# Kernel tuning notes

Hardware: AMD Instinct MI355X
Metric: run time of the kernel (lower is better)

## Reference

```python
import jax, jax.numpy as jnp
import numpy as np

N = 8192
D_IN = 32
HIDDEN = [32, 32, 32]   # -> 2 GraphConvolution layers
FC = [32, 1]            # hfc = [32, 32, 1] -> 2 Linear layers


def _uniform(key, shape, stdv):
    return jax.random.uniform(key, shape, jnp.float32, -stdv, stdv)


def setup_inputs() -> dict:
    key = jax.random.key(0)
    ks = jax.random.split(key, 32)
    inp = {}
    inp["V"] = jax.random.normal(ks[0], (N, D_IN), jnp.float32)
    inp["adj"] = jax.random.randint(ks[1], (N, N), 0, 4, jnp.int32)
    # GCN layer params: w1, w2, w3 [in, out], bias [out]; init U(-stdv, stdv), stdv = 1/sqrt(out)
    ki = 2
    for li in range(len(HIDDEN) - 1):
        a, b = HIDDEN[li], HIDDEN[li + 1]
        stdv = 1.0 / np.sqrt(b)
        for wname in ("w1", "w2", "w3"):
            inp[f"{wname}_{li}"] = _uniform(ks[ki], (a, b), stdv); ki += 1
        inp[f"gb_{li}"] = _uniform(ks[ki], (b,), stdv); ki += 1
    # FC params (torch Linear default init: U(-1/sqrt(in), 1/sqrt(in)))
    hfc = [HIDDEN[-1]] + FC
    for li in range(len(hfc) - 1):
        a, b = hfc[li], hfc[li + 1]
        stdv = 1.0 / np.sqrt(a)
        inp[f"fcW_{li}"] = _uniform(ks[ki], (b, a), stdv); ki += 1  # torch Linear weight is [out, in]
        inp[f"fcb_{li}"] = _uniform(ks[ki], (b,), stdv); ki += 1
    return inp


def _gcn(V, adj, w1, w2, w3, bias):
    # masked-adjacency relational aggregation: sum_k (adj==k) @ (V @ w_k)
    dt = V.dtype
    o = (adj == 1).astype(dt) @ (V @ w1)
    o = o + (adj == 2).astype(dt) @ (V @ w2)
    o = o + (adj == 3).astype(dt) @ (V @ w3)
    return jax.nn.relu(o + bias)


def reference(V, adj, w1_0, w2_0, w3_0, gb_0, w1_1, w2_1, w3_1, gb_1,
              fcW_0, fcb_0, fcW_1, fcb_1):
    Z = _gcn(V, adj, w1_0, w2_0, w3_0, gb_0)          # [N, 32]
    Z = _gcn(Z, adj, w1_1, w2_1, w3_1, gb_1)          # [N, 32]
    Z = jnp.sum(Z, axis=0)                             # [32] sum pooling over nodes
    Z = jax.nn.relu(Z @ fcW_0.T + fcb_0)               # dropout = identity (eval mode)
    Z = Z @ fcW_1.T + fcb_1                            # [1]
    return jax.nn.sigmoid(Z)
```

## Files before the change

kernel.cpp:

```cpp
#include <hip/hip_runtime.h>
#include <cmath>

#define NN 8192

typedef _Float16 half8 __attribute__((ext_vector_type(8)));
typedef float floatx4 __attribute__((ext_vector_type(4)));
typedef unsigned int uint;

template <int L2>
__global__ __launch_bounds__(256) void h_kernel(
    const float* __restrict__ X, const float* __restrict__ w1,
    const float* __restrict__ w2, const float* __restrict__ w3,
    const float* __restrict__ gbias, _Float16* __restrict__ Hfrag) {
  __shared__ float wl[32][32];
  __shared__ float Xs[64][32];
  const int tid = threadIdx.x;
  const int ch = blockIdx.y;
  const float* wsrc = (ch == 0) ? w1 : (ch == 1) ? w2 : w3;
  for (int i = tid; i < 1024; i += 256) ((float*)wl)[i] = wsrc[i];
  const size_t base = (size_t)blockIdx.x * 2048 + tid * 8;
  if (L2 == 0) {
    float4 x0 = ((const float4*)(X + base))[0];
    float4 x1 = ((const float4*)(X + base))[1];
    *((float4*)(&Xs[0][0] + tid * 8)) = x0;
    *((float4*)(&Xs[0][0] + tid * 8 + 4)) = x1;
  } else {
    float4 s0 = {0.f, 0.f, 0.f, 0.f}, s1 = {0.f, 0.f, 0.f, 0.f};
#pragma unroll
    for (int c = 0; c < 8; ++c) {
      const float4* p = (const float4*)(X + (size_t)c * NN * 32 + base);
      float4 a = p[0], b = p[1];
      s0.x += a.x; s0.y += a.y; s0.z += a.z; s0.w += a.w;
      s1.x += b.x; s1.y += b.y; s1.z += b.z; s1.w += b.w;
    }
    const int c0 = (tid * 8) & 31;
    const float4 b0 = *(const float4*)(gbias + c0);
    const float4 b1 = *(const float4*)(gbias + c0 + 4);
    s0.x += b0.x; s0.y += b0.y; s0.z += b0.z; s0.w += b0.w;
    s1.x += b1.x; s1.y += b1.y; s1.z += b1.z; s1.w += b1.w;
    s0.x = s0.x > 0.f ? s0.x : 0.f; s0.y = s0.y > 0.f ? s0.y : 0.f;
    s0.z = s0.z > 0.f ? s0.z : 0.f; s0.w = s0.w > 0.f ? s0.w : 0.f;
    s1.x = s1.x > 0.f ? s1.x : 0.f; s1.y = s1.y > 0.f ? s1.y : 0.f;
    s1.z = s1.z > 0.f ? s1.z : 0.f; s1.w = s1.w > 0.f ? s1.w : 0.f;
    *((float4*)(&Xs[0][0] + tid * 8)) = s0;
    *((float4*)(&Xs[0][0] + tid * 8 + 4)) = s1;
  }
  __syncthreads();
  const int n = tid & 31, jb = tid >> 5;
  const int j0 = blockIdx.x * 64 + jb * 8;
  const int t = j0 >> 5;
  const int lane = (n & 15) | (((j0 & 31) >> 3) << 4);
  const int tile = n >> 4;
  half8 hv;
#pragma unroll
  for (int jj = 0; jj < 8; ++jj) {
    const float4* xr = (const float4*)(&Xs[jb * 8 + jj][0]);
    float acc = 0.f;
#pragma unroll
    for (int d4 = 0; d4 < 8; ++d4) {
      float4 x = xr[d4];
      acc += x.x * wl[d4 * 4 + 0][n];
      acc += x.y * wl[d4 * 4 + 1][n];
      acc += x.z * wl[d4 * 4 + 2][n];
      acc += x.w * wl[d4 * 4 + 3][n];
    }
    hv[jj] = (_Float16)acc;
  }
  size_t idx = ((((size_t)ch * 256 + t) * 2 + tile) * 64 + lane) * 8;
  *(half8*)(Hfrag + idx) = hv;
}

__device__ __forceinline__ void agg_phaseB(const uint* ptile, float* red_raw,
                                           const half8* __restrict__ Hf,
                                           float* __restrict__ Zpart, int rg,
                                           int c, int tid) {
  const int w = tid >> 6, lane = tid & 63;
  const int m = lane & 15, q = lane >> 4;
  uint mk[8];
  *(uint4*)(mk) = *(const uint4*)(ptile + (w * 2) * 256 + lane * 4);
  *(uint4*)(mk + 4) = *(const uint4*)(ptile + (w * 2 + 1) * 256 + lane * 4);
  __syncthreads();
  floatx4 acc00 = {0.f, 0.f, 0.f, 0.f}, acc01 = {0.f, 0.f, 0.f, 0.f};
  floatx4 acc10 = {0.f, 0.f, 0.f, 0.f}, acc11 = {0.f, 0.f, 0.f, 0.f};
#pragma unroll 2
  for (int tl = 0; tl < 8; ++tl) {
    const int t = c * 32 + w * 8 + tl;
    const size_t hb = (size_t)t * 128 + lane;
    half8 b00 = Hf[hb],          b01 = Hf[hb + 64];
    half8 b10 = Hf[hb + 32768],  b11 = Hf[hb + 32768 + 64];
    half8 b20 = Hf[hb + 65536],  b21 = Hf[hb + 65536 + 64];
    const uint pk = mk[tl];
    half8 a1r0, a2r0, a3r0, a1r1, a2r1, a3r1;
#pragma unroll
    for (int i = 0; i < 8; ++i) {
      const int p0 = (pk >> (2 * i)) & 3;
      const int p1 = (pk >> (16 + 2 * i)) & 3;
      a1r0[i] = (p0 == 1) ? (_Float16)1.f : (_Float16)0.f;
      a2r0[i] = (p0 == 2) ? (_Float16)1.f : (_Float16)0.f;
      a3r0[i] = (p0 == 3) ? (_Float16)1.f : (_Float16)0.f;
      a1r1[i] = (p1 == 1) ? (_Float16)1.f : (_Float16)0.f;
      a2r1[i] = (p1 == 2) ? (_Float16)1.f : (_Float16)0.f;
      a3r1[i] = (p1 == 3) ? (_Float16)1.f : (_Float16)0.f;
    }
    acc00 = __builtin_amdgcn_mfma_f32_16x16x32_f16(a1r0, b00, acc00, 0, 0, 0);
    acc00 = __builtin_amdgcn_mfma_f32_16x16x32_f16(a2r0, b10, acc00, 0, 0, 0);
    acc00 = __builtin_amdgcn_mfma_f32_16x16x32_f16(a3r0, b20, acc00, 0, 0, 0);
    acc01 = __builtin_amdgcn_mfma_f32_16x16x32_f16(a1r0, b01, acc01, 0, 0, 0);
    acc01 = __builtin_amdgcn_mfma_f32_16x16x32_f16(a2r0, b11, acc01, 0, 0, 0);
    acc01 = __builtin_amdgcn_mfma_f32_16x16x32_f16(a3r0, b21, acc01, 0, 0, 0);
    acc10 = __builtin_amdgcn_mfma_f32_16x16x32_f16(a1r1, b00, acc10, 0, 0, 0);
    acc10 = __builtin_amdgcn_mfma_f32_16x16x32_f16(a2r1, b10, acc10, 0, 0, 0);
    acc10 = __builtin_amdgcn_mfma_f32_16x16x32_f16(a3r1, b20, acc10, 0, 0, 0);
    acc11 = __builtin_amdgcn_mfma_f32_16x16x32_f16(a1r1, b01, acc11, 0, 0, 0);
    acc11 = __builtin_amdgcn_mfma_f32_16x16x32_f16(a2r1, b11, acc11, 0, 0, 0);
    acc11 = __builtin_amdgcn_mfma_f32_16x16x32_f16(a3r1, b21, acc11, 0, 0, 0);
  }
  float (*red)[4][64][4] = (float (*)[4][64][4])red_raw;
#pragma unroll
  for (int r = 0; r < 4; ++r) {
    red[w][0][lane][r] = acc00[r];
    red[w][1][lane][r] = acc01[r];
    red[w][2][lane][r] = acc10[r];
    red[w][3][lane][r] = acc11[r];
  }
  __syncthreads();
  if (w == 0) {
    const int rbase = rg * 32;
#pragma unroll
    for (int r = 0; r < 4; ++r) {
      const float c00 = red[0][0][lane][r] + red[1][0][lane][r] +
                        red[2][0][lane][r] + red[3][0][lane][r];
      const float c01 = red[0][1][lane][r] + red[1][1][lane][r] +
                        red[2][1][lane][r] + red[3][1][lane][r];
      const float c10 = red[0][2][lane][r] + red[1][2][lane][r] +
                        red[2][2][lane][r] + red[3][2][lane][r];
      const float c11 = red[0][3][lane][r] + red[1][3][lane][r] +
                        red[2][3][lane][r] + red[3][3][lane][r];
      const int ro0 = rbase + q * 4 + r;
      float* zp0 = Zpart + ((size_t)c * NN + ro0) * 32;
      zp0[m] = c00;
      zp0[16 + m] = c01;
      float* zp1 = Zpart + ((size_t)c * NN + ro0 + 16) * 32;
      zp1[m] = c10;
      zp1[16 + m] = c11;
    }
  }
}

__global__ __launch_bounds__(256, 8) void agg_kernel(
    const int* __restrict__ adj, const half8* __restrict__ Hf,
    float* __restrict__ Zpart) {
  __shared__ char smraw[16384];
  uint* ptile = (uint*)smraw;
  const int tid = threadIdx.x;
  const int rg = blockIdx.x >> 3, c = blockIdx.x & 7;
  const int tg = tid >> 5;
  const int qt = (tid >> 1) & 3;
  const int t4 = (tid >> 3) & 3;
  const int ih = tid & 1;
  const int byte_base = tg * 1024 + qt * 256 + t4 * 4 + ih;
  unsigned char* pb = (unsigned char*)ptile;
  const size_t gofs = (size_t)rg * 32 * NN + c * 1024 + tid * 4;
#pragma unroll
  for (int r0 = 0; r0 < 32; r0 += 8) {
    int4 a[8];
#pragma unroll
    for (int rr = 0; rr < 8; ++rr)
      a[rr] = *(const int4*)(adj + gofs + (size_t)(r0 + rr) * NN);
#pragma unroll
    for (int rr = 0; rr < 8; ++rr) {
      const int r = r0 + rr;
      const uint b = (uint)(a[rr].x & 3) | ((uint)(a[rr].y & 3) << 2) |
                     ((uint)(a[rr].z & 3) << 4) | ((uint)(a[rr].w & 3) << 6);
      pb[byte_base + (r & 15) * 16 + (r >> 4) * 2] = (unsigned char)b;
    }
  }
  __syncthreads();
  agg_phaseB(ptile, (float*)smraw, Hf, Zpart, rg, c, tid);
}

__global__ __launch_bounds__(256) void pool_kernel(
    const float* __restrict__ Zpart, const float* __restrict__ bias,
    float* __restrict__ partials) {
  const int tid = threadIdx.x;
  const int col = tid & 31, ro = tid >> 5;
  const float b = bias[col];
  float s = 0.f;
  for (int rr = 0; rr < 32; ++rr) {
    const size_t r = (size_t)blockIdx.x * 256 + ro * 32 + rr;
    float v = b;
#pragma unroll
    for (int c = 0; c < 8; ++c) v += Zpart[(size_t)c * NN * 32 + r * 32 + col];
    s += v > 0.f ? v : 0.f;
  }
  __shared__ float red[8][32];
  red[ro][col] = s;
  __syncthreads();
  if (tid < 32) {
    float t = 0.f;
#pragma unroll
    for (int i = 0; i < 8; ++i) t += red[i][tid];
    partials[(size_t)blockIdx.x * 32 + tid] = t;
  }
}

__global__ __launch_bounds__(256) void fc_kernel(
    const float* __restrict__ partials, int np, const float* __restrict__ W0,
    const float* __restrict__ b0, const float* __restrict__ W1,
    const float* __restrict__ b1, float* __restrict__ out) {
  __shared__ float acc8[8][32];
  __shared__ float z[32], y[32];
  const int tid = threadIdx.x;
  const int col = tid & 31, ch = tid >> 5;
  float s = 0.f;
  for (int i = ch; i < np; i += 8) s += partials[(size_t)i * 32 + col];
  acc8[ch][col] = s;
  __syncthreads();
  if (tid < 32) {
    float t = 0.f;
#pragma unroll
    for (int i = 0; i < 8; ++i) t += acc8[i][tid];
    z[tid] = t;
  }
  __syncthreads();
  if (tid < 32) {
    float acc = b0[tid];
    for (int n = 0; n < 32; ++n) acc += W0[tid * 32 + n] * z[n];
    y[tid] = acc > 0.f ? acc : 0.f;
  }
  __syncthreads();
  if (tid == 0) {
    float acc = b1[0];
    for (int mm = 0; mm < 32; ++mm) acc += W1[mm] * y[mm];
    out[0] = 1.f / (1.f + expf(-acc));
  }
}

extern "C" void kernel_launch(void* const* d_in, const int* in_sizes, int n_in,
                              void* d_out, int out_size, void* d_ws,
                              size_t ws_size, hipStream_t stream) {
  const float* V   = (const float*)d_in[0];
  const int*   adj = (const int*)d_in[1];
  const float *w10 = (const float*)d_in[2], *w20 = (const float*)d_in[3],
              *w30 = (const float*)d_in[4], *gb0 = (const float*)d_in[5];
  const float *w11 = (const float*)d_in[6], *w21 = (const float*)d_in[7],
              *w31 = (const float*)d_in[8], *gb1 = (const float*)d_in[9];
  const float *fW0 = (const float*)d_in[10], *fb0 = (const float*)d_in[11],
              *fW1 = (const float*)d_in[12], *fb1 = (const float*)d_in[13];
  float* out = (float*)d_out;
  char* ws = (char*)d_ws;

  _Float16* Hfrag    = (_Float16*)ws;
  float*    Zpart    = (float*)(ws + 1572864);
  float*    partials = (float*)(ws + 9961472);

  h_kernel<0><<<dim3(128, 3), 256, 0, stream>>>(V, w10, w20, w30, nullptr,
                                                Hfrag);
  agg_kernel<<<2048, 256, 0, stream>>>(adj, (const half8*)Hfrag, Zpart);
  h_kernel<1><<<dim3(128, 3), 256, 0, stream>>>(Zpart, w11, w21, w31, gb0,
                                                Hfrag);
  agg_kernel<<<2048, 256, 0, stream>>>(adj, (const half8*)Hfrag, Zpart);
  pool_kernel<<<32, 256, 0, stream>>>(Zpart, gb1, partials);
  fc_kernel<<<1, 256, 0, stream>>>(partials, 32, fW0, fb0, fW1, fb1, out);
}
```

Measured before the change: 487.1 us.

## Pack adjacency once in first aggregation and reuse packed masks in second layer

```diff
diff --git a/kernel.cpp b/kernel.cpp
--- a/kernel.cpp
+++ b/kernel.cpp
@@ -70,25 +70,28 @@
   *(half8*)(Hfrag + idx) = hv;
 }
 
-__device__ __forceinline__ void agg_phaseB(const uint* ptile, float* red_raw,
-                                           const half8* __restrict__ Hf,
-                                           float* __restrict__ Zpart, int rg,
-                                           int c, int tid) {
+__device__ __forceinline__ void phaseB_core(const uint* mk,
+                                            const half8* __restrict__ Hf,
+                                            float* red_raw,
+                                            float* __restrict__ Zpart, int rg,
+                                            int c, int tid) {
   const int w = tid >> 6, lane = tid & 63;
   const int m = lane & 15, q = lane >> 4;
-  uint mk[8];
-  *(uint4*)(mk) = *(const uint4*)(ptile + (w * 2) * 256 + lane * 4);
-  *(uint4*)(mk + 4) = *(const uint4*)(ptile + (w * 2 + 1) * 256 + lane * 4);
-  __syncthreads();
+  const half8* hp = Hf + (size_t)(c * 32 + w * 8) * 128 + lane;
+  half8 b00 = hp[0],     b01 = hp[64];
+  half8 b10 = hp[32768], b11 = hp[32768 + 64];
+  half8 b20 = hp[65536], b21 = hp[65536 + 64];
   floatx4 acc00 = {0.f, 0.f, 0.f, 0.f}, acc01 = {0.f, 0.f, 0.f, 0.f};
   floatx4 acc10 = {0.f, 0.f, 0.f, 0.f}, acc11 = {0.f, 0.f, 0.f, 0.f};
-#pragma unroll 2
+#pragma unroll
   for (int tl = 0; tl < 8; ++tl) {
-    const int t = c * 32 + w * 8 + tl;
-    const size_t hb = (size_t)t * 128 + lane;
-    half8 b00 = Hf[hb],          b01 = Hf[hb + 64];
-    half8 b10 = Hf[hb + 32768],  b11 = Hf[hb + 32768 + 64];
-    half8 b20 = Hf[hb + 65536],  b21 = Hf[hb + 65536 + 64];
+    half8 n00, n01, n10, n11, n20, n21;
+    if (tl < 7) {
+      const half8* np = hp + (tl + 1) * 128;
+      n00 = np[0];     n01 = np[64];
+      n10 = np[32768]; n11 = np[32768 + 64];
+      n20 = np[65536]; n21 = np[65536 + 64];
+    }
     const uint pk = mk[tl];
     half8 a1r0, a2r0, a3r0, a1r1, a2r1, a3r1;
 #pragma unroll
@@ -114,6 +117,9 @@
     acc11 = __builtin_amdgcn_mfma_f32_16x16x32_f16(a1r1, b01, acc11, 0, 0, 0);
     acc11 = __builtin_amdgcn_mfma_f32_16x16x32_f16(a2r1, b11, acc11, 0, 0, 0);
     acc11 = __builtin_amdgcn_mfma_f32_16x16x32_f16(a3r1, b21, acc11, 0, 0, 0);
+    if (tl < 7) {
+      b00 = n00; b01 = n01; b10 = n10; b11 = n11; b20 = n20; b21 = n21;
+    }
   }
   float (*red)[4][64][4] = (float (*)[4][64][4])red_raw;
 #pragma unroll
@@ -147,9 +153,9 @@
   }
 }
 
-__global__ __launch_bounds__(256, 8) void agg_kernel(
-    const int* __restrict__ adj, const half8* __restrict__ Hf,
-    float* __restrict__ Zpart) {
+__global__ __launch_bounds__(256, 4) void agg1_kernel(
+    const int* __restrict__ adj, uint* __restrict__ packed_g,
+    const half8* __restrict__ Hf, float* __restrict__ Zpart) {
   __shared__ char smraw[16384];
   uint* ptile = (uint*)smraw;
   const int tid = threadIdx.x;
@@ -176,7 +182,30 @@
     }
   }
   __syncthreads();
-  agg_phaseB(ptile, (float*)smraw, Hf, Zpart, rg, c, tid);
+  uint* pg = packed_g + (size_t)blockIdx.x * 2048;
+  *(uint4*)(pg + tid * 8) = *(const uint4*)(ptile + tid * 8);
+  *(uint4*)(pg + tid * 8 + 4) = *(const uint4*)(ptile + tid * 8 + 4);
+  const int w = tid >> 6, lane = tid & 63;
+  uint mk[8];
+  *(uint4*)(mk) = *(const uint4*)(ptile + (w * 2) * 256 + lane * 4);
+  *(uint4*)(mk + 4) = *(const uint4*)(ptile + (w * 2 + 1) * 256 + lane * 4);
+  __syncthreads();
+  phaseB_core(mk, Hf, (float*)smraw, Zpart, rg, c, tid);
+}
+
+__global__ __launch_bounds__(256, 4) void agg2_kernel(
+    const uint* __restrict__ packed_g, const half8* __restrict__ Hf,
+    float* __restrict__ Zpart) {
+  __shared__ float red_lds[4][4][64][4];
+  const int tid = threadIdx.x;
+  const int rg = blockIdx.x >> 3, c = blockIdx.x & 7;
+  const int w = tid >> 6, lane = tid & 63;
+  const uint* pg =
+      packed_g + (size_t)blockIdx.x * 2048 + (w * 2) * 256 + lane * 4;
+  uint mk[8];
+  *(uint4*)(mk) = *(const uint4*)(pg);
+  *(uint4*)(mk + 4) = *(const uint4*)(pg + 256);
+  phaseB_core(mk, Hf, (float*)red_lds, Zpart, rg, c, tid);
 }
 
 __global__ __launch_bounds__(256) void pool_kernel(
@@ -253,13 +282,15 @@
   _Float16* Hfrag    = (_Float16*)ws;
   float*    Zpart    = (float*)(ws + 1572864);
   float*    partials = (float*)(ws + 9961472);
+  uint*     packed   = (uint*)(ws + 10223616);
 
   h_kernel<0><<<dim3(128, 3), 256, 0, stream>>>(V, w10, w20, w30, nullptr,
                                                 Hfrag);
-  agg_kernel<<<2048, 256, 0, stream>>>(adj, (const half8*)Hfrag, Zpart);
+  agg1_kernel<<<2048, 256, 0, stream>>>(adj, packed, (const half8*)Hfrag,
+                                        Zpart);
   h_kernel<1><<<dim3(128, 3), 256, 0, stream>>>(Zpart, w11, w21, w31, gb0,
                                                 Hfrag);
-  agg_kernel<<<2048, 256, 0, stream>>>(adj, (const half8*)Hfrag, Zpart);
+  agg2_kernel<<<2048, 256, 0, stream>>>(packed, (const half8*)Hfrag, Zpart);
   pool_kernel<<<32, 256, 0, stream>>>(Zpart, gb1, partials);
   fc_kernel<<<1, 256, 0, stream>>>(partials, 32, fW0, fb0, fW1, fb1, out);
 }
```

Result: faster. 440.4 us (-9.6%).

## Pack adjacency once to 2-bit global buffer and reuse it across both GCN layers

Applied to the files above, without the earlier changes.

```diff
diff --git a/kernel.cpp b/kernel.cpp
--- a/kernel.cpp
+++ b/kernel.cpp
@@ -7,11 +7,10 @@
 typedef float floatx4 __attribute__((ext_vector_type(4)));
 typedef unsigned int uint;
 
-template <int L2>
 __global__ __launch_bounds__(256) void h_kernel(
     const float* __restrict__ X, const float* __restrict__ w1,
     const float* __restrict__ w2, const float* __restrict__ w3,
-    const float* __restrict__ gbias, _Float16* __restrict__ Hfrag) {
+    _Float16* __restrict__ Hfrag) {
   __shared__ float wl[32][32];
   __shared__ float Xs[64][32];
   const int tid = threadIdx.x;
@@ -19,38 +18,16 @@
   const float* wsrc = (ch == 0) ? w1 : (ch == 1) ? w2 : w3;
   for (int i = tid; i < 1024; i += 256) ((float*)wl)[i] = wsrc[i];
   const size_t base = (size_t)blockIdx.x * 2048 + tid * 8;
-  if (L2 == 0) {
-    float4 x0 = ((const float4*)(X + base))[0];
-    float4 x1 = ((const float4*)(X + base))[1];
-    *((float4*)(&Xs[0][0] + tid * 8)) = x0;
-    *((float4*)(&Xs[0][0] + tid * 8 + 4)) = x1;
-  } else {
-    float4 s0 = {0.f, 0.f, 0.f, 0.f}, s1 = {0.f, 0.f, 0.f, 0.f};
-#pragma unroll
-    for (int c = 0; c < 8; ++c) {
-      const float4* p = (const float4*)(X + (size_t)c * NN * 32 + base);
-      float4 a = p[0], b = p[1];
-      s0.x += a.x; s0.y += a.y; s0.z += a.z; s0.w += a.w;
-      s1.x += b.x; s1.y += b.y; s1.z += b.z; s1.w += b.w;
-    }
-    const int c0 = (tid * 8) & 31;
-    const float4 b0 = *(const float4*)(gbias + c0);
-    const float4 b1 = *(const float4*)(gbias + c0 + 4);
-    s0.x += b0.x; s0.y += b0.y; s0.z += b0.z; s0.w += b0.w;
-    s1.x += b1.x; s1.y += b1.y; s1.z += b1.z; s1.w += b1.w;
-    s0.x = s0.x > 0.f ? s0.x : 0.f; s0.y = s0.y > 0.f ? s0.y : 0.f;
-    s0.z = s0.z > 0.f ? s0.z : 0.f; s0.w = s0.w > 0.f ? s0.w : 0.f;
-    s1.x = s1.x > 0.f ? s1.x : 0.f; s1.y = s1.y > 0.f ? s1.y : 0.f;
-    s1.z = s1.z > 0.f ? s1.z : 0.f; s1.w = s1.w > 0.f ? s1.w : 0.f;
-    *((float4*)(&Xs[0][0] + tid * 8)) = s0;
-    *((float4*)(&Xs[0][0] + tid * 8 + 4)) = s1;
-  }
+  float4 x0 = ((const float4*)(X + base))[0];
+  float4 x1 = ((const float4*)(X + base))[1];
+  *((float4*)(&Xs[0][0] + tid * 8)) = x0;
+  *((float4*)(&Xs[0][0] + tid * 8 + 4)) = x1;
   __syncthreads();
   const int n = tid & 31, jb = tid >> 5;
   const int j0 = blockIdx.x * 64 + jb * 8;
   const int t = j0 >> 5;
   const int lane = (n & 15) | (((j0 & 31) >> 3) << 4);
-  const int tile = n >> 4;
+  const int h = n >> 4;
   half8 hv;
 #pragma unroll
   for (int jj = 0; jj < 8; ++jj) {
@@ -66,92 +43,13 @@
     }
     hv[jj] = (_Float16)acc;
   }
-  size_t idx = ((((size_t)ch * 256 + t) * 2 + tile) * 64 + lane) * 8;
+  size_t idx = ((((size_t)ch * 256 + t) * 2 + h) * 64 + lane) * 8;
   *(half8*)(Hfrag + idx) = hv;
 }
 
-__device__ __forceinline__ void agg_phaseB(const uint* ptile, float* red_raw,
-                                           const half8* __restrict__ Hf,
-                                           float* __restrict__ Zpart, int rg,
-                                           int c, int tid) {
-  const int w = tid >> 6, lane = tid & 63;
-  const int m = lane & 15, q = lane >> 4;
-  uint mk[8];
-  *(uint4*)(mk) = *(const uint4*)(ptile + (w * 2) * 256 + lane * 4);
-  *(uint4*)(mk + 4) = *(const uint4*)(ptile + (w * 2 + 1) * 256 + lane * 4);
-  __syncthreads();
-  floatx4 acc00 = {0.f, 0.f, 0.f, 0.f}, acc01 = {0.f, 0.f, 0.f, 0.f};
-  floatx4 acc10 = {0.f, 0.f, 0.f, 0.f}, acc11 = {0.f, 0.f, 0.f, 0.f};
-#pragma unroll 2
-  for (int tl = 0; tl < 8; ++tl) {
-    const int t = c * 32 + w * 8 + tl;
-    const size_t hb = (size_t)t * 128 + lane;
-    half8 b00 = Hf[hb],          b01 = Hf[hb + 64];
-    half8 b10 = Hf[hb + 32768],  b11 = Hf[hb + 32768 + 64];
-    half8 b20 = Hf[hb + 65536],  b21 = Hf[hb + 65536 + 64];
-    const uint pk = mk[tl];
-    half8 a1r0, a2r0, a3r0, a1r1, a2r1, a3r1;
-#pragma unroll
-    for (int i = 0; i < 8; ++i) {
-      const int p0 = (pk >> (2 * i)) & 3;
-      const int p1 = (pk >> (16 + 2 * i)) & 3;
-      a1r0[i] = (p0 == 1) ? (_Float16)1.f : (_Float16)0.f;
-      a2r0[i] = (p0 == 2) ? (_Float16)1.f : (_Float16)0.f;
-      a3r0[i] = (p0 == 3) ? (_Float16)1.f : (_Float16)0.f;
-      a1r1[i] = (p1 == 1) ? (_Float16)1.f : (_Float16)0.f;
-      a2r1[i] = (p1 == 2) ? (_Float16)1.f : (_Float16)0.f;
-      a3r1[i] = (p1 == 3) ? (_Float16)1.f : (_Float16)0.f;
-    }
-    acc00 = __builtin_amdgcn_mfma_f32_16x16x32_f16(a1r0, b00, acc00, 0, 0, 0);
-    acc00 = __builtin_amdgcn_mfma_f32_16x16x32_f16(a2r0, b10, acc00, 0, 0, 0);
-    acc00 = __builtin_amdgcn_mfma_f32_16x16x32_f16(a3r0, b20, acc00, 0, 0, 0);
-    acc01 = __builtin_amdgcn_mfma_f32_16x16x32_f16(a1r0, b01, acc01, 0, 0, 0);
-    acc01 = __builtin_amdgcn_mfma_f32_16x16x32_f16(a2r0, b11, acc01, 0, 0, 0);
-    acc01 = __builtin_amdgcn_mfma_f32_16x16x32_f16(a3r0, b21, acc01, 0, 0, 0);
-    acc10 = __builtin_amdgcn_mfma_f32_16x16x32_f16(a1r1, b00, acc10, 0, 0, 0);
-    acc10 = __builtin_amdgcn_mfma_f32_16x16x32_f16(a2r1, b10, acc10, 0, 0, 0);
-    acc10 = __builtin_amdgcn_mfma_f32_16x16x32_f16(a3r1, b20, acc10, 0, 0, 0);
-    acc11 = __builtin_amdgcn_mfma_f32_16x16x32_f16(a1r1, b01, acc11, 0, 0, 0);
-    acc11 = __builtin_amdgcn_mfma_f32_16x16x32_f16(a2r1, b11, acc11, 0, 0, 0);
-    acc11 = __builtin_amdgcn_mfma_f32_16x16x32_f16(a3r1, b21, acc11, 0, 0, 0);
-  }
-  float (*red)[4][64][4] = (float (*)[4][64][4])red_raw;
-#pragma unroll
-  for (int r = 0; r < 4; ++r) {
-    red[w][0][lane][r] = acc00[r];
-    red[w][1][lane][r] = acc01[r];
-    red[w][2][lane][r] = acc10[r];
-    red[w][3][lane][r] = acc11[r];
-  }
-  __syncthreads();
-  if (w == 0) {
-    const int rbase = rg * 32;
-#pragma unroll
-    for (int r = 0; r < 4; ++r) {
-      const float c00 = red[0][0][lane][r] + red[1][0][lane][r] +
-                        red[2][0][lane][r] + red[3][0][lane][r];
-      const float c01 = red[0][1][lane][r] + red[1][1][lane][r] +
-                        red[2][1][lane][r] + red[3][1][lane][r];
-      const float c10 = red[0][2][lane][r] + red[1][2][lane][r] +
-                        red[2][2][lane][r] + red[3][2][lane][r];
-      const float c11 = red[0][3][lane][r] + red[1][3][lane][r] +
-                        red[2][3][lane][r] + red[3][3][lane][r];
-      const int ro0 = rbase + q * 4 + r;
-      float* zp0 = Zpart + ((size_t)c * NN + ro0) * 32;
-      zp0[m] = c00;
-      zp0[16 + m] = c01;
-      float* zp1 = Zpart + ((size_t)c * NN + ro0 + 16) * 32;
-      zp1[m] = c10;
-      zp1[16 + m] = c11;
-    }
-  }
-}
-
-__global__ __launch_bounds__(256, 8) void agg_kernel(
-    const int* __restrict__ adj, const half8* __restrict__ Hf,
-    float* __restrict__ Zpart) {
-  __shared__ char smraw[16384];
-  uint* ptile = (uint*)smraw;
+__global__ __launch_bounds__(256, 8) void pack_kernel(
+    const int* __restrict__ adj, uint* __restrict__ packed_g) {
+  __shared__ uint ptile[2048];
   const int tid = threadIdx.x;
   const int rg = blockIdx.x >> 3, c = blockIdx.x & 7;
   const int tg = tid >> 5;
@@ -176,31 +74,123 @@
     }
   }
   __syncthreads();
-  agg_phaseB(ptile, (float*)smraw, Hf, Zpart, rg, c, tid);
+  uint* pg = packed_g + (size_t)blockIdx.x * 2048;
+  *(uint4*)(pg + tid * 8) = *(const uint4*)(ptile + tid * 8);
+  *(uint4*)(pg + tid * 8 + 4) = *(const uint4*)(ptile + tid * 8 + 4);
+}
+
+__global__ __launch_bounds__(256, 3) void agg_kernel(
+    const uint* __restrict__ packed_g, const half8* __restrict__ Hf,
+    float* __restrict__ Zp) {
+  const int tid = threadIdx.x;
+  const int w = tid >> 6, lane = tid & 63;
+  const int m = lane & 15, q = lane >> 4;
+  const int s = blockIdx.x >> 4, rc = blockIdx.x & 15;
+  const int c = s >> 3, tg = s & 7;
+  const half8* hp = Hf + (size_t)(s * 4) * 128 + lane;
+  half8 B[3][4][2];
+#pragma unroll
+  for (int ch = 0; ch < 3; ++ch)
+#pragma unroll
+    for (int t4 = 0; t4 < 4; ++t4) {
+      B[ch][t4][0] = hp[ch * 32768 + t4 * 128];
+      B[ch][t4][1] = hp[ch * 32768 + t4 * 128 + 64];
+    }
+  const int rg0 = rc * 16 + w * 4;
+  const uint* mbase = packed_g + (size_t)c * 2048 + tg * 256 + lane * 4;
+  uint4 mk = *(const uint4*)(mbase + (size_t)rg0 * 8 * 2048);
+#pragma unroll
+  for (int u = 0; u < 4; ++u) {
+    uint4 mkn;
+    if (u < 3) mkn = *(const uint4*)(mbase + (size_t)(rg0 + u + 1) * 8 * 2048);
+    floatx4 acc[2][2];
+#pragma unroll
+    for (int rh = 0; rh < 2; ++rh)
+#pragma unroll
+      for (int h = 0; h < 2; ++h) acc[rh][h] = (floatx4){0.f, 0.f, 0.f, 0.f};
+    const uint mka[4] = {mk.x, mk.y, mk.z, mk.w};
+#pragma unroll
+    for (int t4 = 0; t4 < 4; ++t4) {
+      const uint pk = mka[t4];
+#pragma unroll
+      for (int ch = 0; ch < 3; ++ch) {
+        half8 a0, a1;
+#pragma unroll
+        for (int i = 0; i < 8; ++i) {
+          a0[i] = (((pk >> (2 * i)) & 3) == ch + 1) ? (_Float16)1.f
+                                                    : (_Float16)0.f;
+          a1[i] = (((pk >> (16 + 2 * i)) & 3) == ch + 1) ? (_Float16)1.f
+                                                         : (_Float16)0.f;
+        }
+        acc[0][0] = __builtin_amdgcn_mfma_f32_16x16x32_f16(a0, B[ch][t4][0],
+                                                           acc[0][0], 0, 0, 0);
+        acc[0][1] = __builtin_amdgcn_mfma_f32_16x16x32_f16(a0, B[ch][t4][1],
+                                                           acc[0][1], 0, 0, 0);
+        acc[1][0] = __builtin_amdgcn_mfma_f32_16x16x32_f16(a1, B[ch][t4][0],
+                                                           acc[1][0], 0, 0, 0);
+        acc[1][1] = __builtin_amdgcn_mfma_f32_16x16x32_f16(a1, B[ch][t4][1],
+                                                           acc[1][1], 0, 0, 0);
+      }
+    }
+    const size_t rowb = (size_t)(rg0 + u) * 32 + q * 4;
+#pragma unroll
+    for (int rh = 0; rh < 2; ++rh)
+#pragma unroll
+      for (int h = 0; h < 2; ++h) {
+        float4 v = {acc[rh][h][0], acc[rh][h][1], acc[rh][h][2], acc[rh][h][3]};
+        *(float4*)(Zp + ((size_t)s * 32 + h * 16 + m) * NN + rowb + rh * 16) =
+            v;
+      }
+    if (u < 3) mk = mkn;
+  }
+}
+
+__global__ __launch_bounds__(256) void zsum_kernel(
+    const float* __restrict__ Zp, const float* __restrict__ bias,
+    float* __restrict__ Z1) {
+  const int t = threadIdx.x;
+  const int rq = t & 7, col = t >> 3;
+  const size_t rb = (size_t)blockIdx.x * 32 + rq * 4;
+  float s0 = 0.f, s1 = 0.f, s2 = 0.f, s3 = 0.f;
+  for (int s = 0; s < 64; ++s) {
+    float4 v = *(const float4*)(Zp + ((size_t)s * 32 + col) * NN + rb);
+    s0 += v.x; s1 += v.y; s2 += v.z; s3 += v.w;
+  }
+  const float b = bias[col];
+  s0 += b; s1 += b; s2 += b; s3 += b;
+  s0 = s0 > 0.f ? s0 : 0.f;
+  s1 = s1 > 0.f ? s1 : 0.f;
+  s2 = s2 > 0.f ? s2 : 0.f;
+  s3 = s3 > 0.f ? s3 : 0.f;
+  Z1[(rb + 0) * 32 + col] = s0;
+  Z1[(rb + 1) * 32 + col] = s1;
+  Z1[(rb + 2) * 32 + col] = s2;
+  Z1[(rb + 3) * 32 + col] = s3;
 }
 
 __global__ __launch_bounds__(256) void pool_kernel(
-    const float* __restrict__ Zpart, const float* __restrict__ bias,
+    const float* __restrict__ Zp, const float* __restrict__ bias,
     float* __restrict__ partials) {
-  const int tid = threadIdx.x;
-  const int col = tid & 31, ro = tid >> 5;
+  const int t = threadIdx.x;
+  const int rq = t & 7, col = t >> 3;
+  const size_t rb = (size_t)blockIdx.x * 32 + rq * 4;
+  float s0 = 0.f, s1 = 0.f, s2 = 0.f, s3 = 0.f;
+  for (int s = 0; s < 64; ++s) {
+    float4 v = *(const float4*)(Zp + ((size_t)s * 32 + col) * NN + rb);
+    s0 += v.x; s1 += v.y; s2 += v.z; s3 += v.w;
+  }
   const float b = bias[col];
-  float s = 0.f;
-  for (int rr = 0; rr < 32; ++rr) {
-    const size_t r = (size_t)blockIdx.x * 256 + ro * 32 + rr;
-    float v = b;
-#pragma unroll
-    for (int c = 0; c < 8; ++c) v += Zpart[(size_t)c * NN * 32 + r * 32 + col];
-    s += v > 0.f ? v : 0.f;
-  }
-  __shared__ float red[8][32];
-  red[ro][col] = s;
-  __syncthreads();
-  if (tid < 32) {
-    float t = 0.f;
-#pragma unroll
-    for (int i = 0; i < 8; ++i) t += red[i][tid];
-    partials[(size_t)blockIdx.x * 32 + tid] = t;
+  s0 += b; s1 += b; s2 += b; s3 += b;
+  float sc = (s0 > 0.f ? s0 : 0.f) + (s1 > 0.f ? s1 : 0.f) +
+             (s2 > 0.f ? s2 : 0.f) + (s3 > 0.f ? s3 : 0.f);
+  __shared__ float red[32][9];
+  red[col][rq] = sc;
+  __syncthreads();
+  if (t < 32) {
+    float acc = 0.f;
+#pragma unroll
+    for (int i = 0; i < 8; ++i) acc += red[t][i];
+    partials[(size_t)blockIdx.x * 32 + t] = acc;
   }
 }
 
@@ -251,15 +241,17 @@
   char* ws = (char*)d_ws;
 
   _Float16* Hfrag    = (_Float16*)ws;
-  float*    Zpart    = (float*)(ws + 1572864);
-  float*    partials = (float*)(ws + 9961472);
-
-  h_kernel<0><<<dim3(128, 3), 256, 0, stream>>>(V, w10, w20, w30, nullptr,
-                                                Hfrag);
-  agg_kernel<<<2048, 256, 0, stream>>>(adj, (const half8*)Hfrag, Zpart);
-  h_kernel<1><<<dim3(128, 3), 256, 0, stream>>>(Zpart, w11, w21, w31, gb0,
-                                                Hfrag);
-  agg_kernel<<<2048, 256, 0, stream>>>(adj, (const half8*)Hfrag, Zpart);
-  pool_kernel<<<32, 256, 0, stream>>>(Zpart, gb1, partials);
-  fc_kernel<<<1, 256, 0, stream>>>(partials, 32, fW0, fb0, fW1, fb1, out);
-}
+  float*    Z1       = (float*)(ws + 1572864);
+  float*    partials = (float*)(ws + 2621440);
+  uint*     packed   = (uint*)(ws + 2883584);
+  float*    Zp       = (float*)(ws + 19660800);
+
+  pack_kernel<<<2048, 256, 0, stream>>>(adj, packed);
+  h_kernel<<<dim3(128, 3), 256, 0, stream>>>(V, w10, w20, w30, Hfrag);
+  agg_kernel<<<1024, 256, 0, stream>>>(packed, (const half8*)Hfrag, Zp);
+  zsum_kernel<<<256, 256, 0, stream>>>(Zp, gb0, Z1);
+  h_kernel<<<dim3(128, 3), 256, 0, stream>>>(Z1, w11, w21, w31, Hfrag);
+  agg_kernel<<<1024, 256, 0, stream>>>(packed, (const half8*)Hfrag, Zp);
+  pool_kernel<<<256, 256, 0, stream>>>(Zp, gb1, partials);
+  fc_kernel<<<1, 256, 0, stream>>>(partials, 256, fW0, fb0, fW1, fb1, out);
+}
```

Result: slower. 538.1 us (+10.5%).
